# Kernel tuning notes

Hardware: AMD Instinct MI355X
Metric: run time of the kernel (lower is better)

## Reference

```python
import jax, jax.numpy as jnp
import numpy as np

ORDER = 4          # signature truncation depth
SCALAR_TERM = True # leading 1 term, as in signatory.signature(..., scalar_term=True)
BATCH, STREAM, CHAN = 2048, 128, 5  # channel = path_dim + 1 (time + 4-dim path)


def _exp_levels(dx, m):
    """Tensor exponential of a single increment dx: levels dx^{(x)k}/k!, k=1..m.
    dx: (B, d). Returns list of (B, d**k) arrays."""
    levels = [dx]
    for k in range(2, m + 1):
        prev = levels[-1]  # (B, d**(k-1))
        levels.append((prev[:, :, None] * dx[:, None, :]).reshape(dx.shape[0], -1) / k)
    return levels


def _chen(S, E):
    """Chen's identity: (S tensor-multiply E) truncated to depth m.
    S, E: tuples/lists of (B, d**k) level arrays (level k at list index k-1)."""
    m = len(E)
    B = E[0].shape[0]
    out = []
    for k in range(m):  # output level k+1
        term = S[k] + E[k]
        for i in range(k):  # S level (i+1) tensor E level (k-i)
            a, b = S[i], E[k - 1 - i]
            term = term + (a[:, :, None] * b[:, None, :]).reshape(B, -1)
        out.append(term)
    return tuple(out)


def _signature(path, m, scalar_term):
    """Truncated path signature, flattened levels 1..m (optionally with leading 1).
    path: (B, T, d) -> (B, [1+] d + d^2 + ... + d^m)."""
    B, T, d = path.shape
    dx = jnp.moveaxis(path[:, 1:] - path[:, :-1], 1, 0)  # (T-1, B, d)
    init = tuple(jnp.zeros((B, d ** k), path.dtype) for k in range(1, m + 1))

    def step(S, inc):
        return _chen(S, _exp_levels(inc, m)), None

    S, _ = jax.lax.scan(step, init, dx)
    sig = jnp.concatenate(S, axis=1)
    if scalar_term:
        sig = jnp.concatenate([jnp.ones((B, 1), path.dtype), sig], axis=1)
    return sig


def setup_inputs() -> dict:
    key = jax.random.key(0)
    kx, ky = jax.random.split(key)
    x = jax.random.normal(kx, (BATCH, STREAM, CHAN), dtype=jnp.float32)
    y = jax.random.normal(ky, (BATCH, STREAM, CHAN), dtype=jnp.float32)
    sigma = jnp.ones((CHAN - 1,), dtype=jnp.float32)  # adversarial scaling params
    return {"x": x, "y": y, "sigma": sigma}


def reference(x, y, sigma):
    # adversarial scaling applied to x's non-time channels only (as in forward())
    mu = jnp.concatenate([x[..., :1], x[..., 1:] * sigma], axis=-1)
    nu = y
    # signatures computed once each and shared across kxx, kxy, kyy (same math)
    sx = _signature(mu, ORDER, SCALAR_TERM)  # (B, P)
    sy = _signature(nu, ORDER, SCALAR_TERM)  # (B, P)
    kxx = jnp.einsum('ip,jp->ij', sx, sx)
    kxy = jnp.einsum('ip,jp->ij', sx, sy)
    kyy = jnp.einsum('ip,jp->ij', sy, sy)
    return jnp.mean(kxx) - 2.0 * jnp.mean(kxy) + jnp.mean(kyy)
```

## Files before the change

kernel.cpp:

```cpp
#include <hip/hip_runtime.h>

typedef float v2f __attribute__((ext_vector_type(2)));

#define BATCH  2048
#define TLEN   128
#define CH     5
#define SIGDIM 780
#define NBLK   2048
#define SEGR   32
#define SROW   264
#define RBLK   64
#define ROWSPB (NBLK / RBLK)
#define POISON 0xAAAAAAAAu

__global__ __launch_bounds__(256, 4) void sig_kernel(
    const float* __restrict__ x, const float* __restrict__ y,
    const float* __restrict__ sigma, float* __restrict__ part) {
  const int tid  = threadIdx.x;
  const int wave = tid >> 6;
  const int lane = tid & 63;
  const int h    = lane >> 5;
  const int u    = lane & 31;
  const int q    = wave & 1;
  const int lp   = wave >> 1;
  const bool isX = (blockIdx.x < NBLK / 2);
  const int pbase = (isX ? blockIdx.x : blockIdx.x - NBLK / 2) * 2;
  const int path  = pbase + lp;
  const int segIdx = 2 * q + h;
  const float* src = (isX ? x : y) + (size_t)path * (TLEN * CH) + segIdx * (SEGR * CH);

  __shared__ __align__(16) float segbuf[8][SROW];
  __shared__ float sigbuf[4][SIGDIM];

  const float sg0 = sigma[0], sg1 = sigma[1], sg2 = sigma[2], sg3 = sigma[3];

  float* bw = segbuf[wave * 2 + h];
  if (segIdx == 3 && u < 8) bw[31 * 8 + u] = 0.f;
  const int lim = (segIdx == 3) ? 31 * CH : 32 * CH;
  for (int i = u; i < lim; i += 32) {
    int t = i / CH, c = i - CH * t;
    float v = src[i + CH] - src[i];
    if (isX && c > 0) {
      const float s = (c == 1) ? sg0 : (c == 2) ? sg1 : (c == 3) ? sg2 : sg3;
      v *= s;
    }
    bw[t * 8 + c] = v;
  }
  __syncthreads();

  const int  uc = u < 25 ? u : 24;
  const int  a_ = uc / 5, b_ = uc - 5 * a_;
  const bool act = (u < 25);

  float s1a = 0.f, s2 = 0.f;
  v2f   s3p0 = {0.f, 0.f}, s3p1 = {0.f, 0.f};
  float s3e = 0.f;
  v2f   s4p0[5] = {{0,0},{0,0},{0,0},{0,0},{0,0}};
  v2f   s4p1[5] = {{0,0},{0,0},{0,0},{0,0},{0,0}};
  float s4e[5]  = {0,0,0,0,0};

  const float* pa_ = bw + a_;
  const float* pb_ = bw + b_;

  for (int g = 0; g < 4; ++g) {
    const float* rg = bw + g * 64;
    const float* ra = pa_ + g * 64;
    const float* rb = pb_ + g * 64;
    #pragma unroll
    for (int k = 0; k < 8; ++k) {
      const float4 m = *(const float4*)(rg + k * 8);
      const float d0 = m.x, d1 = m.y, d2 = m.z, d3 = m.w;
      const float d4 = rg[k * 8 + 4];
      const float da = ra[k * 8];
      const float db = rb[k * 8];
      const float pa = s1a * (1.f / 6.f) + da * (1.f / 24.f);
      const float qa = s1a * 0.5f        + da * (1.f / 6.f);
      const float rr = s1a               + da * 0.5f;
      s1a += da;
      const float p2 = 0.5f * s2 + db * pa;
      const float q2 =        s2 + db * qa;
      s2 += db * rr;
      const v2f dc01 = {d0, d1};
      const v2f dc23 = {d2, d3};
      const v2f p2v  = {p2, p2};
      const v2f q2v  = {q2, q2};
      const v2f p30  = __builtin_elementwise_fma(dc01, p2v, s3p0);
      const v2f p31  = __builtin_elementwise_fma(dc23, p2v, s3p1);
      const float p3e = s3e + d4 * p2;
      s3p0 = __builtin_elementwise_fma(dc01, q2v, s3p0);
      s3p1 = __builtin_elementwise_fma(dc23, q2v, s3p1);
      s3e += d4 * q2;
      #pragma unroll
      for (int d = 0; d < 5; ++d) {
        const float dd = (d == 0) ? d0 : (d == 1) ? d1 : (d == 2) ? d2 : (d == 3) ? d3 : d4;
        const v2f ddv = {dd, dd};
        s4p0[d] = __builtin_elementwise_fma(ddv, p30, s4p0[d]);
        s4p1[d] = __builtin_elementwise_fma(ddv, p31, s4p1[d]);
        s4e[d] += dd * p3e;
      }
    }
  }

  float S3[5] = {s3p0.x, s3p0.y, s3p1.x, s3p1.y, s3e};
  float S4[5][5];
  #pragma unroll
  for (int d = 0; d < 5; ++d) {
    S4[0][d] = s4p0[d].x; S4[1][d] = s4p0[d].y;
    S4[2][d] = s4p1[d].x; S4[3][d] = s4p1[d].y;
    S4[4][d] = s4e[d];
  }

  if (h == 1 && act) {
    float* sgb = sigbuf[wave];
    if (b_ == 0) sgb[a_] = s1a;
    sgb[5 + uc] = s2;
    #pragma unroll
    for (int c = 0; c < 5; ++c) {
      sgb[30 + uc * 5 + c] = S3[c];
      #pragma unroll
      for (int d = 0; d < 5; ++d) sgb[155 + (uc * 5 + c) * 5 + d] = S4[c][d];
    }
  }
  __syncthreads();

  float o1 = 0.f, o2 = 0.f, o3[5], o4[5][5];
  if (h == 0 && act) {
    const float* R = sigbuf[wave];
    o1 = s1a + R[a_];
    o2 = s2 + s1a * R[b_] + R[5 + uc];
    #pragma unroll
    for (int c = 0; c < 5; ++c) {
      o3[c] = S3[c] + s2 * R[c] + s1a * R[5 + b_ * 5 + c] + R[30 + uc * 5 + c];
      #pragma unroll
      for (int d = 0; d < 5; ++d)
        o4[c][d] = S4[c][d] + S3[c] * R[d] + s2 * R[5 + c * 5 + d]
                 + s1a * R[30 + (b_ * 5 + c) * 5 + d]
                 + R[155 + (uc * 5 + c) * 5 + d];
    }
  }
  __syncthreads();

  if (h == 0 && act) {
    float* sgb = sigbuf[wave];
    if (b_ == 0) sgb[a_] = o1;
    sgb[5 + uc] = o2;
    #pragma unroll
    for (int c = 0; c < 5; ++c) {
      sgb[30 + uc * 5 + c] = o3[c];
      #pragma unroll
      for (int d = 0; d < 5; ++d) sgb[155 + (uc * 5 + c) * 5 + d] = o4[c][d];
    }
  }
  __syncthreads();

  const int pl = tid >> 7;
  const int t2 = tid & 127;
  float f1v = 0.f, f2v = 0.f, f3v = 0.f, f4v[5] = {0, 0, 0, 0, 0};
  if (t2 < 125) {
    const float* L  = sigbuf[2 * pl];
    const float* Rr = sigbuf[2 * pl + 1];
    const int abq = t2 / 5, c = t2 - 5 * abq;
    const int a = abq / 5, b = abq - 5 * a;
    const float l1 = L[a], l2 = L[5 + abq], l3 = L[30 + t2];
    f3v = l3 + Rr[30 + t2] + l2 * Rr[c] + l1 * Rr[5 + b * 5 + c];
    #pragma unroll
    for (int d = 0; d < 5; ++d)
      f4v[d] = L[155 + t2 * 5 + d] + Rr[155 + t2 * 5 + d]
             + l3 * Rr[d] + l2 * Rr[5 + c * 5 + d]
             + l1 * Rr[30 + (b * 5 + c) * 5 + d];
    if (t2 < 25) {
      const int aa = t2 / 5, bb = t2 - 5 * aa;
      f2v = L[5 + t2] + Rr[5 + t2] + L[aa] * Rr[bb];
    }
    if (t2 < 5) f1v = L[t2] + Rr[t2];
  }

  float* blockAcc = (float*)segbuf;
  if (pl == 0 && t2 < 125) {
    blockAcc[30 + t2] = f3v;
    #pragma unroll
    for (int d = 0; d < 5; ++d) blockAcc[155 + t2 * 5 + d] = f4v[d];
    if (t2 < 25) blockAcc[5 + t2] = f2v;
    if (t2 < 5)  blockAcc[t2] = f1v;
  }
  __syncthreads();
  if (pl == 1 && t2 < 125) {
    blockAcc[30 + t2] += f3v;
    #pragma unroll
    for (int d = 0; d < 5; ++d) blockAcc[155 + t2 * 5 + d] += f4v[d];
    if (t2 < 25) blockAcc[5 + t2] += f2v;
    if (t2 < 5)  blockAcc[t2] += f1v;
  }
  __syncthreads();

  const float w = isX ? 1.0f : -1.0f;
  float* pp = part + (size_t)blockIdx.x * SIGDIM;
  for (int i = tid; i < SIGDIM; i += 256) pp[i] = w * blockAcc[i];
}

__global__ __launch_bounds__(256) void red_kernel(
    const float* __restrict__ part, float* __restrict__ acc2,
    unsigned int* __restrict__ counter, float* __restrict__ out) {
  const int tid = threadIdx.x;
  if (tid < SIGDIM / 4) {
    float4 s = {0.f, 0.f, 0.f, 0.f};
    const float* base = part + (size_t)blockIdx.x * ROWSPB * SIGDIM + 4 * tid;
    #pragma unroll 8
    for (int r = 0; r < ROWSPB; ++r) {
      const float4 v = *(const float4*)(base + (size_t)r * SIGDIM);
      s.x += v.x; s.y += v.y; s.z += v.z; s.w += v.w;
    }
    atomicAdd(&acc2[4 * tid + 0], s.x);
    atomicAdd(&acc2[4 * tid + 1], s.y);
    atomicAdd(&acc2[4 * tid + 2], s.z);
    atomicAdd(&acc2[4 * tid + 3], s.w);
  }

  __shared__ float red[4];
  __shared__ unsigned int lastFlag;
  __syncthreads();
  if (tid == 0) {
    __threadfence();
    unsigned int old = __hip_atomic_fetch_add(counter, 1u, __ATOMIC_ACQ_REL,
                                              __HIP_MEMORY_SCOPE_AGENT);
    lastFlag = (old == POISON + (RBLK - 1)) ? 1u : 0u;
  }
  __syncthreads();
  if (lastFlag) {
    float local = 0.f;
    if (tid < SIGDIM / 4) {
      float vx = __hip_atomic_load(&acc2[4 * tid + 0], __ATOMIC_RELAXED, __HIP_MEMORY_SCOPE_AGENT);
      float vy = __hip_atomic_load(&acc2[4 * tid + 1], __ATOMIC_RELAXED, __HIP_MEMORY_SCOPE_AGENT);
      float vz = __hip_atomic_load(&acc2[4 * tid + 2], __ATOMIC_RELAXED, __HIP_MEMORY_SCOPE_AGENT);
      float vw = __hip_atomic_load(&acc2[4 * tid + 3], __ATOMIC_RELAXED, __HIP_MEMORY_SCOPE_AGENT);
      local = vx * vx + vy * vy + vz * vz + vw * vw;
    }
    #pragma unroll
    for (int off = 32; off > 0; off >>= 1) local += __shfl_down(local, off, 64);
    if ((tid & 63) == 0) red[tid >> 6] = local;
    __syncthreads();
    if (tid == 0)
      out[0] = (red[0] + red[1] + red[2] + red[3]) / (2048.0f * 2048.0f);
  }
}

extern "C" void kernel_launch(void* const* d_in, const int* in_sizes, int n_in,
                              void* d_out, int out_size, void* d_ws, size_t ws_size,
                              hipStream_t stream) {
  const float* x     = (const float*)d_in[0];
  const float* y     = (const float*)d_in[1];
  const float* sigma = (const float*)d_in[2];
  float* out = (float*)d_out;
  float* part = (float*)d_ws;
  float* acc2 = (float*)((char*)d_ws + (size_t)NBLK * SIGDIM * sizeof(float));
  unsigned int* counter =
      (unsigned int*)((char*)d_ws + (size_t)NBLK * SIGDIM * sizeof(float)
                      + SIGDIM * sizeof(float));

  sig_kernel<<<dim3(NBLK), dim3(256), 0, stream>>>(x, y, sigma, part);
  red_kernel<<<dim3(RBLK), dim3(256), 0, stream>>>(part, acc2, counter, out);
}
```

Baseline: 98.13 us.

## Fuse reduction into signature kernel, one wave per path with 2 segments

Each wave now processes a whole path split into two 64-step halves instead of four 32-step segments, so blocks hold four paths and the grid halves. Block-wide barriers between segment merges become wave barriers. The separate reduction kernel is removed: blocks atomically add their summed signatures into 64 spread accumulator rows, and the last block to finish reduces those rows and computes the output. Some scalar FMAs in the inner recurrence are packed into v2f operations. Longer sequential scans per lane mean less parallelism, and atomic contention replaces the partial-buffer write.

```diff
diff --git a/kernel.cpp b/kernel.cpp
--- a/kernel.cpp
+++ b/kernel.cpp
@@ -6,37 +6,35 @@
 #define TLEN   128
 #define CH     5
 #define SIGDIM 780
-#define NBLK   2048
-#define SEGR   32
-#define SROW   264
-#define RBLK   64
-#define ROWSPB (NBLK / RBLK)
+#define NBLK   1024
+#define SROW   520
+#define ROWS   64
 #define POISON 0xAAAAAAAAu
 
 __global__ __launch_bounds__(256, 4) void sig_kernel(
     const float* __restrict__ x, const float* __restrict__ y,
-    const float* __restrict__ sigma, float* __restrict__ part) {
+    const float* __restrict__ sigma, float* __restrict__ acc,
+    unsigned int* __restrict__ counter, float* __restrict__ out) {
   const int tid  = threadIdx.x;
   const int wave = tid >> 6;
   const int lane = tid & 63;
   const int h    = lane >> 5;
   const int u    = lane & 31;
-  const int q    = wave & 1;
-  const int lp   = wave >> 1;
   const bool isX = (blockIdx.x < NBLK / 2);
-  const int pbase = (isX ? blockIdx.x : blockIdx.x - NBLK / 2) * 2;
-  const int path  = pbase + lp;
-  const int segIdx = 2 * q + h;
-  const float* src = (isX ? x : y) + (size_t)path * (TLEN * CH) + segIdx * (SEGR * CH);
+  const int pbase = (isX ? blockIdx.x : blockIdx.x - NBLK / 2) * 4;
+  const int path  = pbase + wave;
+  const float* src = (isX ? x : y) + (size_t)path * (TLEN * CH) + h * (64 * CH);
 
   __shared__ __align__(16) float segbuf[8][SROW];
   __shared__ float sigbuf[4][SIGDIM];
+  __shared__ float redbuf[4];
+  __shared__ unsigned int lastFlag;
 
   const float sg0 = sigma[0], sg1 = sigma[1], sg2 = sigma[2], sg3 = sigma[3];
 
   float* bw = segbuf[wave * 2 + h];
-  if (segIdx == 3 && u < 8) bw[31 * 8 + u] = 0.f;
-  const int lim = (segIdx == 3) ? 31 * CH : 32 * CH;
+  if (h == 1 && u < 8) bw[63 * 8 + u] = 0.f;
+  const int lim = (h == 1) ? 63 * CH : 64 * CH;
   for (int i = u; i < lim; i += 32) {
     int t = i / CH, c = i - CH * t;
     float v = src[i + CH] - src[i];
@@ -46,7 +44,7 @@
     }
     bw[t * 8 + c] = v;
   }
-  __syncthreads();
+  __builtin_amdgcn_wave_barrier();
 
   const int  uc = u < 25 ? u : 24;
   const int  a_ = uc / 5, b_ = uc - 5 * a_;
@@ -57,12 +55,13 @@
   float s3e = 0.f;
   v2f   s4p0[5] = {{0,0},{0,0},{0,0},{0,0},{0,0}};
   v2f   s4p1[5] = {{0,0},{0,0},{0,0},{0,0},{0,0}};
-  float s4e[5]  = {0,0,0,0,0};
+  v2f   s4e01 = {0.f, 0.f}, s4e23 = {0.f, 0.f};
+  float s4e4 = 0.f;
 
   const float* pa_ = bw + a_;
   const float* pb_ = bw + b_;
 
-  for (int g = 0; g < 4; ++g) {
+  for (int g = 0; g < 8; ++g) {
     const float* rg = bw + g * 64;
     const float* ra = pa_ + g * 64;
     const float* rb = pb_ + g * 64;
@@ -73,31 +72,39 @@
       const float d4 = rg[k * 8 + 4];
       const float da = ra[k * 8];
       const float db = rb[k * 8];
-      const float pa = s1a * (1.f / 6.f) + da * (1.f / 24.f);
-      const float qa = s1a * 0.5f        + da * (1.f / 6.f);
-      const float rr = s1a               + da * 0.5f;
-      s1a += da;
-      const float p2 = 0.5f * s2 + db * pa;
-      const float q2 =        s2 + db * qa;
-      s2 += db * rr;
+      const v2f dav = {da, da}, dbv = {db, db}, d4v = {d4, d4};
+      const v2f pq = __builtin_elementwise_fma(
+          dav, (v2f){1.f / 24.f, 1.f / 6.f},
+          (v2f){s1a, s1a} * (v2f){1.f / 6.f, 0.5f});
+      const v2f rs = __builtin_elementwise_fma(dav, (v2f){0.5f, 1.f},
+                                               (v2f){s1a, s1a});
+      const float rr = rs.x;
+      s1a = rs.y;
+      const v2f p2q2 = __builtin_elementwise_fma(
+          dbv, pq, (v2f){s2, s2} * (v2f){0.5f, 1.f});
+      s2 = __builtin_fmaf(db, rr, s2);
+      const float p2 = p2q2.x, q2 = p2q2.y;
       const v2f dc01 = {d0, d1};
       const v2f dc23 = {d2, d3};
-      const v2f p2v  = {p2, p2};
-      const v2f q2v  = {q2, q2};
-      const v2f p30  = __builtin_elementwise_fma(dc01, p2v, s3p0);
-      const v2f p31  = __builtin_elementwise_fma(dc23, p2v, s3p1);
-      const float p3e = s3e + d4 * p2;
+      const v2f p2v = {p2, p2}, q2v = {q2, q2};
+      const v2f p30 = __builtin_elementwise_fma(dc01, p2v, s3p0);
+      const v2f p31 = __builtin_elementwise_fma(dc23, p2v, s3p1);
+      const v2f pe = __builtin_elementwise_fma(d4v, p2q2, (v2f){s3e, s3e});
+      const float p3e = pe.x;
+      s3e = pe.y;
       s3p0 = __builtin_elementwise_fma(dc01, q2v, s3p0);
       s3p1 = __builtin_elementwise_fma(dc23, q2v, s3p1);
-      s3e += d4 * q2;
+      const v2f p3ev = {p3e, p3e};
       #pragma unroll
       for (int d = 0; d < 5; ++d) {
         const float dd = (d == 0) ? d0 : (d == 1) ? d1 : (d == 2) ? d2 : (d == 3) ? d3 : d4;
         const v2f ddv = {dd, dd};
         s4p0[d] = __builtin_elementwise_fma(ddv, p30, s4p0[d]);
         s4p1[d] = __builtin_elementwise_fma(ddv, p31, s4p1[d]);
-        s4e[d] += dd * p3e;
       }
+      s4e01 = __builtin_elementwise_fma(dc01, p3ev, s4e01);
+      s4e23 = __builtin_elementwise_fma(dc23, p3ev, s4e23);
+      s4e4 = __builtin_fmaf(d4, p3e, s4e4);
     }
   }
 
@@ -107,8 +114,9 @@
   for (int d = 0; d < 5; ++d) {
     S4[0][d] = s4p0[d].x; S4[1][d] = s4p0[d].y;
     S4[2][d] = s4p1[d].x; S4[3][d] = s4p1[d].y;
-    S4[4][d] = s4e[d];
-  }
+  }
+  S4[4][0] = s4e01.x; S4[4][1] = s4e01.y;
+  S4[4][2] = s4e23.x; S4[4][3] = s4e23.y; S4[4][4] = s4e4;
 
   if (h == 1 && act) {
     float* sgb = sigbuf[wave];
@@ -121,13 +129,13 @@
       for (int d = 0; d < 5; ++d) sgb[155 + (uc * 5 + c) * 5 + d] = S4[c][d];
     }
   }
-  __syncthreads();
-
-  float o1 = 0.f, o2 = 0.f, o3[5], o4[5][5];
+  __builtin_amdgcn_wave_barrier();
+
   if (h == 0 && act) {
     const float* R = sigbuf[wave];
-    o1 = s1a + R[a_];
-    o2 = s2 + s1a * R[b_] + R[5 + uc];
+    float o3[5], o4[5][5];
+    const float o1 = s1a + R[a_];
+    const float o2 = s2 + s1a * R[b_] + R[5 + uc];
     #pragma unroll
     for (int c = 0; c < 5; ++c) {
       o3[c] = S3[c] + s2 * R[c] + s1a * R[5 + b_ * 5 + c] + R[30 + uc * 5 + c];
@@ -137,10 +145,6 @@
                  + s1a * R[30 + (b_ * 5 + c) * 5 + d]
                  + R[155 + (uc * 5 + c) * 5 + d];
     }
-  }
-  __syncthreads();
-
-  if (h == 0 && act) {
     float* sgb = sigbuf[wave];
     if (b_ == 0) sgb[a_] = o1;
     sgb[5 + uc] = o2;
@@ -151,96 +155,41 @@
       for (int d = 0; d < 5; ++d) sgb[155 + (uc * 5 + c) * 5 + d] = o4[c][d];
     }
   }
+
   __syncthreads();
-
-  const int pl = tid >> 7;
-  const int t2 = tid & 127;
-  float f1v = 0.f, f2v = 0.f, f3v = 0.f, f4v[5] = {0, 0, 0, 0, 0};
-  if (t2 < 125) {
-    const float* L  = sigbuf[2 * pl];
-    const float* Rr = sigbuf[2 * pl + 1];
-    const int abq = t2 / 5, c = t2 - 5 * abq;
-    const int a = abq / 5, b = abq - 5 * a;
-    const float l1 = L[a], l2 = L[5 + abq], l3 = L[30 + t2];
-    f3v = l3 + Rr[30 + t2] + l2 * Rr[c] + l1 * Rr[5 + b * 5 + c];
-    #pragma unroll
-    for (int d = 0; d < 5; ++d)
-      f4v[d] = L[155 + t2 * 5 + d] + Rr[155 + t2 * 5 + d]
-             + l3 * Rr[d] + l2 * Rr[5 + c * 5 + d]
-             + l1 * Rr[30 + (b * 5 + c) * 5 + d];
-    if (t2 < 25) {
-      const int aa = t2 / 5, bb = t2 - 5 * aa;
-      f2v = L[5 + t2] + Rr[5 + t2] + L[aa] * Rr[bb];
-    }
-    if (t2 < 5) f1v = L[t2] + Rr[t2];
-  }
-
-  float* blockAcc = (float*)segbuf;
-  if (pl == 0 && t2 < 125) {
-    blockAcc[30 + t2] = f3v;
-    #pragma unroll
-    for (int d = 0; d < 5; ++d) blockAcc[155 + t2 * 5 + d] = f4v[d];
-    if (t2 < 25) blockAcc[5 + t2] = f2v;
-    if (t2 < 5)  blockAcc[t2] = f1v;
+  const float w = isX ? 1.0f : -1.0f;
+  float* accrow = acc + (size_t)(blockIdx.x & (ROWS - 1)) * SIGDIM;
+  for (int i = tid; i < SIGDIM; i += 256) {
+    const float s = sigbuf[0][i] + sigbuf[1][i] + sigbuf[2][i] + sigbuf[3][i];
+    atomicAdd(&accrow[i], w * s);
   }
   __syncthreads();
-  if (pl == 1 && t2 < 125) {
-    blockAcc[30 + t2] += f3v;
-    #pragma unroll
-    for (int d = 0; d < 5; ++d) blockAcc[155 + t2 * 5 + d] += f4v[d];
-    if (t2 < 25) blockAcc[5 + t2] += f2v;
-    if (t2 < 5)  blockAcc[t2] += f1v;
-  }
-  __syncthreads();
-
-  const float w = isX ? 1.0f : -1.0f;
-  float* pp = part + (size_t)blockIdx.x * SIGDIM;
-  for (int i = tid; i < SIGDIM; i += 256) pp[i] = w * blockAcc[i];
-}
-
-__global__ __launch_bounds__(256) void red_kernel(
-    const float* __restrict__ part, float* __restrict__ acc2,
-    unsigned int* __restrict__ counter, float* __restrict__ out) {
-  const int tid = threadIdx.x;
-  if (tid < SIGDIM / 4) {
-    float4 s = {0.f, 0.f, 0.f, 0.f};
-    const float* base = part + (size_t)blockIdx.x * ROWSPB * SIGDIM + 4 * tid;
-    #pragma unroll 8
-    for (int r = 0; r < ROWSPB; ++r) {
-      const float4 v = *(const float4*)(base + (size_t)r * SIGDIM);
-      s.x += v.x; s.y += v.y; s.z += v.z; s.w += v.w;
-    }
-    atomicAdd(&acc2[4 * tid + 0], s.x);
-    atomicAdd(&acc2[4 * tid + 1], s.y);
-    atomicAdd(&acc2[4 * tid + 2], s.z);
-    atomicAdd(&acc2[4 * tid + 3], s.w);
-  }
-
-  __shared__ float red[4];
-  __shared__ unsigned int lastFlag;
-  __syncthreads();
+
   if (tid == 0) {
     __threadfence();
     unsigned int old = __hip_atomic_fetch_add(counter, 1u, __ATOMIC_ACQ_REL,
                                               __HIP_MEMORY_SCOPE_AGENT);
-    lastFlag = (old == POISON + (RBLK - 1)) ? 1u : 0u;
+    lastFlag = (old == POISON + (NBLK - 1)) ? 1u : 0u;
   }
   __syncthreads();
+
   if (lastFlag) {
     float local = 0.f;
-    if (tid < SIGDIM / 4) {
-      float vx = __hip_atomic_load(&acc2[4 * tid + 0], __ATOMIC_RELAXED, __HIP_MEMORY_SCOPE_AGENT);
-      float vy = __hip_atomic_load(&acc2[4 * tid + 1], __ATOMIC_RELAXED, __HIP_MEMORY_SCOPE_AGENT);
-      float vz = __hip_atomic_load(&acc2[4 * tid + 2], __ATOMIC_RELAXED, __HIP_MEMORY_SCOPE_AGENT);
-      float vw = __hip_atomic_load(&acc2[4 * tid + 3], __ATOMIC_RELAXED, __HIP_MEMORY_SCOPE_AGENT);
-      local = vx * vx + vy * vy + vz * vz + vw * vw;
+    for (int c = tid; c < SIGDIM; c += 256) {
+      float uacc = 0.f;
+      #pragma unroll 16
+      for (int r = 0; r < ROWS; ++r)
+        uacc += __hip_atomic_load(&acc[(size_t)r * SIGDIM + c],
+                                  __ATOMIC_RELAXED, __HIP_MEMORY_SCOPE_AGENT);
+      local += uacc * uacc;
     }
     #pragma unroll
     for (int off = 32; off > 0; off >>= 1) local += __shfl_down(local, off, 64);
-    if ((tid & 63) == 0) red[tid >> 6] = local;
+    if ((tid & 63) == 0) redbuf[tid >> 6] = local;
     __syncthreads();
     if (tid == 0)
-      out[0] = (red[0] + red[1] + red[2] + red[3]) / (2048.0f * 2048.0f);
+      out[0] = (redbuf[0] + redbuf[1] + redbuf[2] + redbuf[3])
+             * (1.0f / (2048.0f * 2048.0f));
   }
 }
 
@@ -251,12 +200,9 @@
   const float* y     = (const float*)d_in[1];
   const float* sigma = (const float*)d_in[2];
   float* out = (float*)d_out;
-  float* part = (float*)d_ws;
-  float* acc2 = (float*)((char*)d_ws + (size_t)NBLK * SIGDIM * sizeof(float));
+  float* acc = (float*)d_ws;
   unsigned int* counter =
-      (unsigned int*)((char*)d_ws + (size_t)NBLK * SIGDIM * sizeof(float)
-                      + SIGDIM * sizeof(float));
-
-  sig_kernel<<<dim3(NBLK), dim3(256), 0, stream>>>(x, y, sigma, part);
-  red_kernel<<<dim3(RBLK), dim3(256), 0, stream>>>(part, acc2, counter, out);
+      (unsigned int*)((char*)d_ws + (size_t)ROWS * SIGDIM * sizeof(float));
+
+  sig_kernel<<<dim3(NBLK), dim3(256), 0, stream>>>(x, y, sigma, acc, counter, out);
 }
```

After: 113.9 us. +16.1%, slower.
